# Optimization experiments

Hardware: AMD Instinct MI355X
Metric: run time of the kernel (lower is better)

## Reference

```python
import jax, jax.numpy as jnp
import numpy as np

N_NODES = 100000
N_EDGES = 1600000
N_GRAPHS = 64
NUM_FEATURES = 512
NUM_CLASSES = 10


def setup_inputs() -> dict:
    key = jax.random.key(0)
    ks = jax.random.split(key, 8)
    x = jax.random.normal(ks[0], (N_NODES, NUM_FEATURES), dtype=jnp.float32)
    edge_index = jax.random.randint(ks[1], (2, N_EDGES), 0, N_NODES, dtype=jnp.int32)
    batch = jnp.sort(jax.random.randint(ks[2], (N_NODES,), 0, N_GRAPHS, dtype=jnp.int32))
    def init_w(k, fin, fout):
        return jax.random.normal(k, (fin, fout), dtype=jnp.float32) * (1.0 / np.sqrt(fin))
    W1 = init_w(ks[3], NUM_FEATURES, 128)
    W2 = init_w(ks[4], 128, 64)
    W3 = init_w(ks[5], 64, 32)
    Wfc = init_w(ks[6], 32, NUM_CLASSES)
    return {
        "x": x, "edge_index": edge_index, "batch": batch,
        "W1": W1, "b1": jnp.zeros((128,), jnp.float32),
        "W2": W2, "b2": jnp.zeros((64,), jnp.float32),
        "W3": W3, "b3": jnp.zeros((32,), jnp.float32),
        "Wfc": Wfc, "bfc": jnp.zeros((NUM_CLASSES,), jnp.float32),
    }


def _gcn_conv(x, src, dst, norm, W, b):
    # PyG GCNConv: linear first, then normalized neighbor aggregation (with self-loops), then bias.
    h = x @ W                                   # [N, F_out]
    msg = norm[:, None] * h[src]                # gather + scale, [E+N, F_out]
    out = jnp.zeros_like(h).at[dst].add(msg)    # scatter-add to targets
    return out + b


def reference(x, edge_index, batch, W1, b1, W2, b2, W3, b3, Wfc, bfc):
    n = x.shape[0]
    loops = jnp.arange(n, dtype=edge_index.dtype)
    src = jnp.concatenate([edge_index[0], loops])  # source nodes (+ self-loops)
    dst = jnp.concatenate([edge_index[1], loops])  # target nodes (+ self-loops)
    # symmetric normalization D^{-1/2} (A+I) D^{-1/2}; degrees counted at targets
    deg = jnp.zeros((n,), x.dtype).at[dst].add(1.0)
    dinv = jnp.where(deg > 0, jax.lax.rsqrt(deg), 0.0)
    norm = dinv[src] * dinv[dst]                # [E+N]

    h = jax.nn.relu(_gcn_conv(x, src, dst, norm, W1, b1))   # dropout is identity in eval
    h = jax.nn.relu(_gcn_conv(h, src, dst, norm, W2, b2))
    h = jax.nn.relu(_gcn_conv(h, src, dst, norm, W3, b3))

    pooled = jax.ops.segment_max(h, batch, num_segments=N_GRAPHS)  # global max pool per graph
    logits = pooled @ Wfc + bfc
    return jax.nn.log_softmax(logits, axis=1)
```

## Files before the change

kernel.cpp:

```cpp
#include <hip/hip_runtime.h>
#include <hip/hip_bf16.h>


typedef __attribute__((ext_vector_type(8))) short short8;
typedef __attribute__((ext_vector_type(8))) unsigned short ushort8v;
typedef __attribute__((ext_vector_type(4))) float f32x4;

constexpr int NB   = 1024;
constexpr int CAPB = 4096;
constexpr int EPB  = 6400;

__device__ __forceinline__ unsigned short f2bf(float f) {
    __hip_bfloat16 h = __float2bfloat16(f);
    return *(unsigned short*)&h;
}
__device__ __forceinline__ float bfu2f(unsigned short u) {
    unsigned int v = ((unsigned int)u) << 16;
    return __uint_as_float(v);
}

__global__ void setup_kernel(const float* __restrict__ W1, const float* __restrict__ W2,
                             const float* __restrict__ W3,
                             unsigned short* __restrict__ Wt1, unsigned short* __restrict__ Wt2,
                             unsigned short* __restrict__ Wt3,
                             int* __restrict__ bcnt, float* __restrict__ pooled) {
    int t = blockIdx.x * 256 + threadIdx.x;
    if (t < NB * 16) bcnt[t] = 0;
    if (t < 64 * 32) pooled[t] = 0.0f;
    if (t < 128 * 512) {
        int n = t >> 9, k = t & 511;
        Wt1[t] = f2bf(W1[(size_t)k * 128 + n]);
    } else if (t < 128 * 512 + 64 * 128) {
        int u = t - 128 * 512;
        int n = u >> 7, k = u & 127;
        Wt2[u] = f2bf(W2[(size_t)k * 64 + n]);
    } else if (t < 128 * 512 + 64 * 128 + 32 * 64) {
        int u = t - (128 * 512 + 64 * 128);
        int n = u >> 6, k = u & 63;
        Wt3[u] = f2bf(W3[(size_t)k * 32 + n]);
    }
}

__global__ __launch_bounds__(256) void partition_edges(
        const int* __restrict__ src, const int* __restrict__ dst,
        int* __restrict__ bcnt, unsigned* __restrict__ bucketed, int E) {
    __shared__ unsigned h[NB], rs[NB], cur[NB], gs[NB];
    __shared__ unsigned wtot[4];
    __shared__ unsigned ebuf[EPB];
    __shared__ unsigned short ebkt[EPB];

    const int t = threadIdx.x;
    const int e0 = blockIdx.x * EPB;
    const int nloc = min(EPB, E - e0);

    for (int i = t; i < NB; i += 256) h[i] = 0;
    __syncthreads();

    for (int i = t; i < nloc; i += 256) {
        int d = dst[e0 + i];
        atomicAdd(&h[d >> 7], 1u);
    }
    __syncthreads();

    const unsigned b0 = 4u * t;
    unsigned s0 = h[b0], s1 = h[b0 + 1], s2 = h[b0 + 2], s3 = h[b0 + 3];
    unsigned tsum = s0 + s1 + s2 + s3;
    unsigned scan = tsum;
#pragma unroll
    for (int off = 1; off < 64; off <<= 1) {
        unsigned v = __shfl_up(scan, off, 64);
        if ((t & 63) >= off) scan += v;
    }
    if ((t & 63) == 63) wtot[t >> 6] = scan;
    __syncthreads();
    unsigned woff = 0;
    for (int w = 0; w < (t >> 6); ++w) woff += wtot[w];
    unsigned excl = woff + scan - tsum;
    rs[b0] = excl;                    cur[b0] = excl;
    rs[b0 + 1] = excl + s0;           cur[b0 + 1] = excl + s0;
    rs[b0 + 2] = excl + s0 + s1;      cur[b0 + 2] = excl + s0 + s1;
    rs[b0 + 3] = excl + s0 + s1 + s2; cur[b0 + 3] = excl + s0 + s1 + s2;
    if (s0) gs[b0]     = (unsigned)atomicAdd(&bcnt[(b0) * 16], (int)s0);
    if (s1) gs[b0 + 1] = (unsigned)atomicAdd(&bcnt[(b0 + 1) * 16], (int)s1);
    if (s2) gs[b0 + 2] = (unsigned)atomicAdd(&bcnt[(b0 + 2) * 16], (int)s2);
    if (s3) gs[b0 + 3] = (unsigned)atomicAdd(&bcnt[(b0 + 3) * 16], (int)s3);
    __syncthreads();

    for (int i = t; i < nloc; i += 256) {
        int d = dst[e0 + i];
        int s = src[e0 + i];
        int b = d >> 7;
        unsigned p = atomicAdd(&cur[b], 1u);
        ebuf[p] = ((unsigned)s << 7) | (unsigned)(d & 127);
        ebkt[p] = (unsigned short)b;
    }
    __syncthreads();

    for (int p = t; p < nloc; p += 256) {
        unsigned v = ebuf[p];
        int b = ebkt[p];
        unsigned g = gs[b] + ((unsigned)p - rs[b]);
        if (g < CAPB) bucketed[(size_t)b * CAPB + g] = v;
    }
}

__global__ __launch_bounds__(256) void bucket_csr(
        const unsigned* __restrict__ bucketed, const int* __restrict__ bcnt,
        int* __restrict__ cnt, int* __restrict__ slab, float* __restrict__ dinv, int N) {
    __shared__ int lcnt[128];
    __shared__ unsigned lslab[128 * 64];

    const int b = blockIdx.x;
    const int t = threadIdx.x;
    if (t < 128) lcnt[t] = 0;
    __syncthreads();

    int nE = bcnt[b * 16];
    if (nE > CAPB) nE = CAPB;
    const unsigned* bb = bucketed + (size_t)b * CAPB;
    for (int e = t; e < nE; e += 256) {
        unsigned v = bb[e];
        int ln = v & 127;
        int pos = atomicAdd(&lcnt[ln], 1);
        if (pos < 64) lslab[ln * 64 + pos] = v >> 7;
    }
    __syncthreads();

    const int node0 = b * 128;
    const int nnodes = min(128, N - node0);
    if (nnodes <= 0) return;
    const int tot4 = (nnodes * 64) / 4;
    int4* gout = (int4*)&slab[(size_t)node0 * 64];
    const int4* lin = (const int4*)lslab;
    for (int i = t; i < tot4; i += 256) gout[i] = lin[i];
    if (t < nnodes) {
        int deg = lcnt[t];
        cnt[node0 + t] = deg;
        dinv[node0 + t] = rsqrtf(1.0f + (float)deg);
    }
}

template <int NOUT, bool A_BF16>
__global__ __launch_bounds__(256) void mfma_gemm(
        const float* __restrict__ Af, const unsigned short* __restrict__ Ab,
        const unsigned short* __restrict__ Wt, const float* __restrict__ dinv,
        unsigned short* __restrict__ C, int M, int K) {
    constexpr int NT = NOUT / 16;
    constexpr int CH = 136;

    __shared__ short As[16 * CH];
    __shared__ short Bs[NT * 4 * CH];

    const int t = threadIdx.x;
    const int w = t >> 6;
    const int lane = t & 63;
    const int row0 = blockIdx.x * 64;

    f32x4 acc[NT];
#pragma unroll
    for (int c = 0; c < NT; ++c) acc[c] = (f32x4){0.f, 0.f, 0.f, 0.f};

    const int ar = t >> 2;
    const int aq = t & 3;
    const int arow = row0 + ar;
    const int a_lds = ((ar >> 4) * 4 + aq) * CH + (ar & 15) * 8;

    const int bn = t >> 1;
    const int bh = t & 1;
    const int b_lds0 = ((bn >> 4) * 4 + 2 * bh) * CH + (bn & 15) * 8;

    for (int k0 = 0; k0 < K; k0 += 32) {
        short8 apack;
        if (A_BF16) {
            if (arow < M) apack = *(const short8*)&Ab[(size_t)arow * K + k0 + aq * 8];
            else apack = (short8){0, 0, 0, 0, 0, 0, 0, 0};
        } else {
            float4 u0 = make_float4(0.f, 0.f, 0.f, 0.f), u1 = u0;
            if (arow < M) {
                const float* ap = Af + (size_t)arow * K + k0 + aq * 8;
                u0 = *(const float4*)ap;
                u1 = *(const float4*)(ap + 4);
            }
            apack[0] = (short)f2bf(u0.x); apack[1] = (short)f2bf(u0.y);
            apack[2] = (short)f2bf(u0.z); apack[3] = (short)f2bf(u0.w);
            apack[4] = (short)f2bf(u1.x); apack[5] = (short)f2bf(u1.y);
            apack[6] = (short)f2bf(u1.z); apack[7] = (short)f2bf(u1.w);
        }
        short8 w0, w1;
        if (t < 2 * NOUT) {
            const unsigned short* wp = Wt + (size_t)bn * K + k0 + 16 * bh;
            w0 = *(const short8*)wp;
            w1 = *(const short8*)(wp + 8);
        }
        __syncthreads();
        *(short8*)&As[a_lds] = apack;
        if (t < 2 * NOUT) {
            *(short8*)&Bs[b_lds0] = w0;
            *(short8*)&Bs[b_lds0 + CH] = w1;
        }
        __syncthreads();

        short8 a = *(short8*)&As[(w * 4 + (lane >> 4)) * CH + (lane & 15) * 8];
#pragma unroll
        for (int c = 0; c < NT; ++c) {
            short8 b = *(short8*)&Bs[(c * 4 + (lane >> 4)) * CH + (lane & 15) * 8];
            acc[c] = __builtin_amdgcn_mfma_f32_16x16x32_bf16(a, b, acc[c], 0, 0, 0);
        }
    }

    const int q = lane >> 4, i = lane & 15;
#pragma unroll
    for (int reg = 0; reg < 4; ++reg) {
        int row = row0 + w * 16 + q * 4 + reg;
        if (row < M) {
            float di = dinv[row];
#pragma unroll
            for (int c = 0; c < NT; ++c)
                C[(size_t)row * NOUT + c * 16 + i] = f2bf(di * acc[c][reg]);
        }
    }
}

template <int F>
__device__ __forceinline__ void gather_acc(
        const int* __restrict__ cnt, const int* __restrict__ slab,
        const unsigned short* __restrict__ hs, int node, size_t fo, float acc[8]) {
    {
        ushort8v s = *(const ushort8v*)&hs[(size_t)node * F + fo];
#pragma unroll
        for (int i = 0; i < 8; ++i) acc[i] = bfu2f(s[i]);
    }
    int deg = cnt[node];
    if (deg > 64) deg = 64;
    const int* sl = slab + (size_t)node * 64;

    int j = 0;
    for (; j + 8 <= deg; j += 8) {
        int4 a4 = *(const int4*)&sl[j];
        int4 b4 = *(const int4*)&sl[j + 4];
        ushort8v v0 = *(const ushort8v*)&hs[(size_t)a4.x * F + fo];
        ushort8v v1 = *(const ushort8v*)&hs[(size_t)a4.y * F + fo];
        ushort8v v2 = *(const ushort8v*)&hs[(size_t)a4.z * F + fo];
        ushort8v v3 = *(const ushort8v*)&hs[(size_t)a4.w * F + fo];
        ushort8v v4 = *(const ushort8v*)&hs[(size_t)b4.x * F + fo];
        ushort8v v5 = *(const ushort8v*)&hs[(size_t)b4.y * F + fo];
        ushort8v v6 = *(const ushort8v*)&hs[(size_t)b4.z * F + fo];
        ushort8v v7 = *(const ushort8v*)&hs[(size_t)b4.w * F + fo];
#pragma unroll
        for (int i = 0; i < 8; ++i)
            acc[i] += ((bfu2f(v0[i]) + bfu2f(v1[i])) + (bfu2f(v2[i]) + bfu2f(v3[i]))) +
                      ((bfu2f(v4[i]) + bfu2f(v5[i])) + (bfu2f(v6[i]) + bfu2f(v7[i])));
    }
    for (; j + 4 <= deg; j += 4) {
        int4 s4 = *(const int4*)&sl[j];
        ushort8v v0 = *(const ushort8v*)&hs[(size_t)s4.x * F + fo];
        ushort8v v1 = *(const ushort8v*)&hs[(size_t)s4.y * F + fo];
        ushort8v v2 = *(const ushort8v*)&hs[(size_t)s4.z * F + fo];
        ushort8v v3 = *(const ushort8v*)&hs[(size_t)s4.w * F + fo];
#pragma unroll
        for (int i = 0; i < 8; ++i)
            acc[i] += (bfu2f(v0[i]) + bfu2f(v1[i])) + (bfu2f(v2[i]) + bfu2f(v3[i]));
    }
    for (; j < deg; ++j) {
        int s = sl[j];
        ushort8v v = *(const ushort8v*)&hs[(size_t)s * F + fo];
#pragma unroll
        for (int i = 0; i < 8; ++i) acc[i] += bfu2f(v[i]);
    }
}

template <int F, int NOUT>
__global__ __launch_bounds__(256) void gather_gemm(
        const int* __restrict__ cnt, const int* __restrict__ slab,
        const float* __restrict__ dinv, const unsigned short* __restrict__ hs,
        const float* __restrict__ bias, const unsigned short* __restrict__ Wt,
        unsigned short* __restrict__ Cout, int N) {
    constexpr int F8 = F / 8;
    constexpr int NPB = 256 / F8;
    constexpr int LDA = F + 8;
    constexpr int MT = NPB / 16;
    constexpr int KS = F / 32;

    __shared__ short At[NPB * LDA];
    __shared__ short Bs[NOUT * LDA];

    const int t = threadIdx.x;
    const int node0 = blockIdx.x * NPB;
    const int nl = t / F8;
    const int lf = t % F8;
    const int node = node0 + nl;
    const size_t fo = (size_t)lf * 8;

#pragma unroll
    for (int idx = t * 8; idx < NOUT * F; idx += 256 * 8) {
        int r = idx / F, k = idx % F;
        *(short8*)&Bs[r * LDA + k] = *(const short8*)&Wt[idx];
    }

    short8 arow = (short8){0, 0, 0, 0, 0, 0, 0, 0};
    if (node < N) {
        float acc[8];
        gather_acc<F>(cnt, slab, hs, node, fo, acc);
        const float di = dinv[node];
#pragma unroll
        for (int i = 0; i < 8; ++i)
            arow[i] = (short)f2bf(fmaxf(di * acc[i] + bias[fo + i], 0.f));
    }
    *(short8*)&At[nl * LDA + lf * 8] = arow;
    __syncthreads();

    const int w = t >> 6, l = t & 63;
    const int m = (MT == 1) ? 0 : (w >> 1);
    const int c = (MT == 1) ? w : (w & 1);
    f32x4 acc4 = (f32x4){0.f, 0.f, 0.f, 0.f};
#pragma unroll
    for (int ks = 0; ks < KS; ++ks) {
        short8 a = *(short8*)&At[(m * 16 + (l & 15)) * LDA + ks * 32 + (l >> 4) * 8];
        short8 b = *(short8*)&Bs[(c * 16 + (l & 15)) * LDA + ks * 32 + (l >> 4) * 8];
        acc4 = __builtin_amdgcn_mfma_f32_16x16x32_bf16(a, b, acc4, 0, 0, 0);
    }
    const int q = l >> 4, i = l & 15;
#pragma unroll
    for (int reg = 0; reg < 4; ++reg) {
        int grow = node0 + m * 16 + q * 4 + reg;
        if (grow < N)
            Cout[(size_t)grow * NOUT + c * 16 + i] = f2bf(dinv[grow] * acc4[reg]);
    }
}

__global__ __launch_bounds__(256) void gather_pool(
        const int* __restrict__ cnt, const int* __restrict__ slab,
        const float* __restrict__ dinv, const unsigned short* __restrict__ hs,
        const float* __restrict__ bias, const int* __restrict__ batch,
        float* __restrict__ pooled, int N) {
    constexpr int F = 32, F8 = 4, NPB = 64;
    __shared__ float P[NPB * 32];
    __shared__ int gbuf[NPB];

    const int t = threadIdx.x;
    const int node0 = blockIdx.x * NPB;
    const int nl = t >> 2, lf = t & 3;
    const int node = node0 + nl;
    const size_t fo = (size_t)lf * 8;

    float ov[8] = {0.f, 0.f, 0.f, 0.f, 0.f, 0.f, 0.f, 0.f};
    if (node < N) {
        float acc[8];
        gather_acc<F>(cnt, slab, hs, node, fo, acc);
        const float di = dinv[node];
#pragma unroll
        for (int i = 0; i < 8; ++i) ov[i] = fmaxf(di * acc[i] + bias[fo + i], 0.f);
    }
#pragma unroll
    for (int i = 0; i < 8; ++i) P[nl * 32 + lf * 8 + i] = ov[i];
    if (t < NPB) gbuf[t] = (node0 + t < N) ? batch[node0 + t] : -1;
    __syncthreads();

    if (t < 32) {
        int gcur = -1;
        float vmax = 0.f;
        for (int j = 0; j < NPB; ++j) {
            int g = gbuf[j];
            if (g < 0) break;
            if (g != gcur) {
                if (gcur >= 0) atomicMax((int*)&pooled[gcur * 32 + t], __float_as_int(vmax));
                gcur = g;
                vmax = 0.f;
            }
            vmax = fmaxf(vmax, P[j * 32 + t]);
        }
        if (gcur >= 0) atomicMax((int*)&pooled[gcur * 32 + t], __float_as_int(vmax));
    }
}

__global__ void head_kernel(const float* __restrict__ pooled, const float* __restrict__ Wfc,
                            const float* __restrict__ bfc, float* __restrict__ out) {
    int g = threadIdx.x;
    float p[32];
#pragma unroll
    for (int f = 0; f < 32; ++f) p[f] = pooled[g * 32 + f];
    float logits[10];
#pragma unroll
    for (int c = 0; c < 10; ++c) {
        float acc = bfc[c];
#pragma unroll
        for (int f = 0; f < 32; ++f) acc += p[f] * Wfc[f * 10 + c];
        logits[c] = acc;
    }
    float m = logits[0];
#pragma unroll
    for (int c = 1; c < 10; ++c) m = fmaxf(m, logits[c]);
    float s = 0.f;
#pragma unroll
    for (int c = 0; c < 10; ++c) s += expf(logits[c] - m);
    float lse = m + logf(s);
#pragma unroll
    for (int c = 0; c < 10; ++c) out[g * 10 + c] = logits[c] - lse;
}

extern "C" void kernel_launch(void* const* d_in, const int* in_sizes, int n_in,
                              void* d_out, int out_size, void* d_ws, size_t ws_size,
                              hipStream_t stream) {
    const float* x   = (const float*)d_in[0];
    const int*   ei  = (const int*)d_in[1];
    const int*   bat = (const int*)d_in[2];
    const float* W1  = (const float*)d_in[3];
    const float* b1  = (const float*)d_in[4];
    const float* W2  = (const float*)d_in[5];
    const float* b2  = (const float*)d_in[6];
    const float* W3  = (const float*)d_in[7];
    const float* b3  = (const float*)d_in[8];
    const float* Wfc = (const float*)d_in[9];
    const float* bfc = (const float*)d_in[10];
    float* out = (float*)d_out;

    const int N = in_sizes[2];
    const int E = in_sizes[1] / 2;
    const int K0 = in_sizes[0] / N;

    const int* src = ei;
    const int* dst = ei + E;

    float* ws = (float*)d_ws;
    float* dinv = ws;
    unsigned short* HS  = (unsigned short*)(ws + N);
    unsigned short* HS2 = HS + (size_t)N * 128;
    unsigned short* HS3 = HS2 + (size_t)N * 64;
    float* pooled = (float*)(HS3 + (size_t)N * 32);
    unsigned short* Wt1 = (unsigned short*)(pooled + 2048);
    unsigned short* Wt2 = Wt1 + 128 * 512;
    unsigned short* Wt3 = Wt2 + 64 * 128;
    int* cnt = (int*)(Wt3 + 32 * 64);
    int* slab = cnt + N;
    int* bcnt = slab + (size_t)N * 64;
    unsigned* bucketed = (unsigned*)(bcnt + NB * 16);

    const int gb = (N + 63) / 64;
    const int NBUCK = (N + 127) >> 7;

    setup_kernel<<<(128 * 512 + 64 * 128 + 32 * 64 + 255) / 256, 256, 0, stream>>>(
        W1, W2, W3, Wt1, Wt2, Wt3, bcnt, pooled);

    partition_edges<<<(E + EPB - 1) / EPB, 256, 0, stream>>>(src, dst, bcnt, bucketed, E);
    bucket_csr<<<NBUCK, 256, 0, stream>>>(bucketed, bcnt, cnt, slab, dinv, N);

    mfma_gemm<128, false><<<gb, 256, 0, stream>>>(x, nullptr, Wt1, dinv, HS, N, K0);

    gather_gemm<128, 64><<<(N + 15) / 16, 256, 0, stream>>>(
        cnt, slab, dinv, HS, b1, Wt2, HS2, N);

    gather_gemm<64, 32><<<(N + 31) / 32, 256, 0, stream>>>(
        cnt, slab, dinv, HS2, b2, Wt3, HS3, N);

    gather_pool<<<(N + 63) / 64, 256, 0, stream>>>(cnt, slab, dinv, HS3, b3, bat, pooled, N);

    head_kernel<<<1, 64, 0, stream>>>(pooled, Wfc, bfc, out);
}
```

Measured before the change: 503.2 us.

## Compact per-node edge lists into packed CSR and halve edges per partition block

Replaces the fixed 64-slot-per-node edge slab with a compacted edge array. Each bucket block runs a prefix scan over padded degrees and claims a global offset with an atomic, and a packed meta word holds the start offset and degree. This cuts the slab write traffic (N*64 ints) and improves locality of edge-index reads in the gather kernels. EPB is also halved so partition_edges launches more blocks. In exchange it adds a shared-memory scan and a serial per-thread copy in bucket_csr, and edge list order across buckets now depends on atomic ordering.

```diff
diff --git a/kernel.cpp b/kernel.cpp
--- a/kernel.cpp
+++ b/kernel.cpp
@@ -8,7 +8,7 @@
 
 constexpr int NB   = 1024;
 constexpr int CAPB = 4096;
-constexpr int EPB  = 6400;
+constexpr int EPB  = 3200;
 
 __device__ __forceinline__ unsigned short f2bf(float f) {
     __hip_bfloat16 h = __float2bfloat16(f);
@@ -23,8 +23,10 @@
                              const float* __restrict__ W3,
                              unsigned short* __restrict__ Wt1, unsigned short* __restrict__ Wt2,
                              unsigned short* __restrict__ Wt3,
-                             int* __restrict__ bcnt, float* __restrict__ pooled) {
+                             int* __restrict__ bcnt, int* __restrict__ gctr,
+                             float* __restrict__ pooled) {
     int t = blockIdx.x * 256 + threadIdx.x;
+    if (t == 0) gctr[0] = 0;
     if (t < NB * 16) bcnt[t] = 0;
     if (t < 64 * 32) pooled[t] = 0.0f;
     if (t < 128 * 512) {
@@ -106,9 +108,12 @@
 
 __global__ __launch_bounds__(256) void bucket_csr(
         const unsigned* __restrict__ bucketed, const int* __restrict__ bcnt,
-        int* __restrict__ cnt, int* __restrict__ slab, float* __restrict__ dinv, int N) {
+        unsigned* __restrict__ meta, int* __restrict__ edges,
+        float* __restrict__ dinv, int* __restrict__ gctr, int N) {
     __shared__ int lcnt[128];
     __shared__ unsigned lslab[128 * 64];
+    __shared__ int loff[128];
+    __shared__ int sbase;
 
     const int b = blockIdx.x;
     const int t = threadIdx.x;
@@ -126,17 +131,35 @@
     }
     __syncthreads();
 
-    const int node0 = b * 128;
-    const int nnodes = min(128, N - node0);
-    if (nnodes <= 0) return;
-    const int tot4 = (nnodes * 64) / 4;
-    int4* gout = (int4*)&slab[(size_t)node0 * 64];
-    const int4* lin = (const int4*)lslab;
-    for (int i = t; i < tot4; i += 256) gout[i] = lin[i];
-    if (t < nnodes) {
-        int deg = lcnt[t];
-        cnt[node0 + t] = deg;
-        dinv[node0 + t] = rsqrtf(1.0f + (float)deg);
+    int rawdeg = 0, deg = 0, pad = 0;
+    if (t < 128) {
+        rawdeg = lcnt[t];
+        deg = min(rawdeg, 64);
+        pad = (deg + 3) & ~3;
+        loff[t] = pad;
+    }
+    __syncthreads();
+#pragma unroll
+    for (int off = 1; off < 128; off <<= 1) {
+        int v = 0;
+        if (t < 128 && t >= off) v = loff[t - off];
+        __syncthreads();
+        if (t < 128) loff[t] += v;
+        __syncthreads();
+    }
+    if (t == 127) sbase = atomicAdd(gctr, loff[127]);
+    __syncthreads();
+
+    if (t < 128) {
+        int node = b * 128 + t;
+        if (node < N) {
+            int start = sbase + loff[t] - pad;
+            meta[node] = ((unsigned)(start >> 2) << 7) | (unsigned)deg;
+            dinv[node] = rsqrtf(1.0f + (float)rawdeg);
+            int4* dp = (int4*)&edges[start];
+            const int4* sp = (const int4*)&lslab[t * 64];
+            for (int i = 0; i < (deg + 3) / 4; ++i) dp[i] = sp[i];
+        }
     }
 }
 
@@ -223,16 +246,16 @@
 
 template <int F>
 __device__ __forceinline__ void gather_acc(
-        const int* __restrict__ cnt, const int* __restrict__ slab,
+        const unsigned* __restrict__ meta, const int* __restrict__ edges,
         const unsigned short* __restrict__ hs, int node, size_t fo, float acc[8]) {
     {
         ushort8v s = *(const ushort8v*)&hs[(size_t)node * F + fo];
 #pragma unroll
         for (int i = 0; i < 8; ++i) acc[i] = bfu2f(s[i]);
     }
-    int deg = cnt[node];
-    if (deg > 64) deg = 64;
-    const int* sl = slab + (size_t)node * 64;
+    const unsigned mv = meta[node];
+    const int deg = (int)(mv & 127u);
+    const int* sl = edges + ((size_t)(mv >> 7) << 2);
 
     int j = 0;
     for (; j + 8 <= deg; j += 8) {
@@ -271,7 +294,7 @@
 
 template <int F, int NOUT>
 __global__ __launch_bounds__(256) void gather_gemm(
-        const int* __restrict__ cnt, const int* __restrict__ slab,
+        const unsigned* __restrict__ meta, const int* __restrict__ edges,
         const float* __restrict__ dinv, const unsigned short* __restrict__ hs,
         const float* __restrict__ bias, const unsigned short* __restrict__ Wt,
         unsigned short* __restrict__ Cout, int N) {
@@ -300,7 +323,7 @@
     short8 arow = (short8){0, 0, 0, 0, 0, 0, 0, 0};
     if (node < N) {
         float acc[8];
-        gather_acc<F>(cnt, slab, hs, node, fo, acc);
+        gather_acc<F>(meta, edges, hs, node, fo, acc);
         const float di = dinv[node];
 #pragma unroll
         for (int i = 0; i < 8; ++i)
@@ -329,7 +352,7 @@
 }
 
 __global__ __launch_bounds__(256) void gather_pool(
-        const int* __restrict__ cnt, const int* __restrict__ slab,
+        const unsigned* __restrict__ meta, const int* __restrict__ edges,
         const float* __restrict__ dinv, const unsigned short* __restrict__ hs,
         const float* __restrict__ bias, const int* __restrict__ batch,
         float* __restrict__ pooled, int N) {
@@ -346,7 +369,7 @@
     float ov[8] = {0.f, 0.f, 0.f, 0.f, 0.f, 0.f, 0.f, 0.f};
     if (node < N) {
         float acc[8];
-        gather_acc<F>(cnt, slab, hs, node, fo, acc);
+        gather_acc<F>(meta, edges, hs, node, fo, acc);
         const float di = dinv[node];
 #pragma unroll
         for (int i = 0; i < 8; ++i) ov[i] = fmaxf(di * acc[i] + bias[fo + i], 0.f);
@@ -430,29 +453,30 @@
     unsigned short* Wt1 = (unsigned short*)(pooled + 2048);
     unsigned short* Wt2 = Wt1 + 128 * 512;
     unsigned short* Wt3 = Wt2 + 64 * 128;
-    int* cnt = (int*)(Wt3 + 32 * 64);
-    int* slab = cnt + N;
-    int* bcnt = slab + (size_t)N * 64;
+    unsigned* meta = (unsigned*)(Wt3 + 32 * 64);
+    int* edges = (int*)(meta + N);
+    int* gctr = edges + (E + 3 * N + 64);
+    int* bcnt = gctr + 16;
     unsigned* bucketed = (unsigned*)(bcnt + NB * 16);
 
     const int gb = (N + 63) / 64;
     const int NBUCK = (N + 127) >> 7;
 
     setup_kernel<<<(128 * 512 + 64 * 128 + 32 * 64 + 255) / 256, 256, 0, stream>>>(
-        W1, W2, W3, Wt1, Wt2, Wt3, bcnt, pooled);
+        W1, W2, W3, Wt1, Wt2, Wt3, bcnt, gctr, pooled);
 
     partition_edges<<<(E + EPB - 1) / EPB, 256, 0, stream>>>(src, dst, bcnt, bucketed, E);
-    bucket_csr<<<NBUCK, 256, 0, stream>>>(bucketed, bcnt, cnt, slab, dinv, N);
+    bucket_csr<<<NBUCK, 256, 0, stream>>>(bucketed, bcnt, meta, edges, dinv, gctr, N);
 
     mfma_gemm<128, false><<<gb, 256, 0, stream>>>(x, nullptr, Wt1, dinv, HS, N, K0);
 
     gather_gemm<128, 64><<<(N + 15) / 16, 256, 0, stream>>>(
-        cnt, slab, dinv, HS, b1, Wt2, HS2, N);
+        meta, edges, dinv, HS, b1, Wt2, HS2, N);
 
     gather_gemm<64, 32><<<(N + 31) / 32, 256, 0, stream>>>(
-        cnt, slab, dinv, HS2, b2, Wt3, HS3, N);
-
-    gather_pool<<<(N + 63) / 64, 256, 0, stream>>>(cnt, slab, dinv, HS3, b3, bat, pooled, N);
+        meta, edges, dinv, HS2, b2, Wt3, HS3, N);
+
+    gather_pool<<<(N + 63) / 64, 256, 0, stream>>>(meta, edges, dinv, HS3, b3, bat, pooled, N);
 
     head_kernel<<<1, 64, 0, stream>>>(pooled, Wfc, bfc, out);
 }
```

New measurement: 512.4 us. About the same (+1.8%).
